# Optimization experiments

Measured on AMD Instinct MI355X. Metric: run time of the kernel, lower is better.

The kernel has to match this reference:

```python
import jax, jax.numpy as jnp
import numpy as np

INPUT_SIZE = 128
HIDDEN_SIZE = 128
B, S = 4, 4096


def setup_inputs() -> dict:
    key = jax.random.key(0)
    ks = jax.random.split(key, 9)
    sc_in = 1.0 / np.sqrt(INPUT_SIZE)
    sc_h = 1.0 / np.sqrt(HIDDEN_SIZE)
    return {
        "x": jax.random.normal(ks[0], (B, S, INPUT_SIZE), jnp.float32),
        "Wq": jax.random.uniform(ks[1], (INPUT_SIZE, HIDDEN_SIZE), jnp.float32, -sc_in, sc_in),
        "bq": jax.random.uniform(ks[2], (HIDDEN_SIZE,), jnp.float32, -sc_in, sc_in),
        "Wk": jax.random.uniform(ks[3], (INPUT_SIZE, HIDDEN_SIZE), jnp.float32, -sc_in, sc_in),
        "bk": jax.random.uniform(ks[4], (HIDDEN_SIZE,), jnp.float32, -sc_in, sc_in),
        "Wv": jax.random.uniform(ks[5], (INPUT_SIZE, HIDDEN_SIZE), jnp.float32, -sc_in, sc_in),
        "bv": jax.random.uniform(ks[6], (HIDDEN_SIZE,), jnp.float32, -sc_in, sc_in),
        "Wo": jax.random.uniform(ks[7], (HIDDEN_SIZE, INPUT_SIZE), jnp.float32, -sc_h, sc_h),
        "bo": jax.random.uniform(ks[8], (INPUT_SIZE,), jnp.float32, -sc_h, sc_h),
    }


def reference(x, Wq, bq, Wk, bk, Wv, bv, Wo, bo):
    # single-head scaled dot-product attention (non-causal), dropout is eval-mode identity
    q = x @ Wq + bq                      # [B, S, H]
    k = x @ Wk + bk                      # [B, S, H]
    v = x @ Wv + bv                      # [B, S, H]
    scale = 1.0 / jnp.sqrt(jnp.asarray(HIDDEN_SIZE, x.dtype))
    scores = jnp.einsum("bsh,bth->bst", q, k) * scale   # [B, S, S]
    attn = jax.nn.softmax(scores, axis=-1)
    attended = jnp.einsum("bst,bth->bsh", attn, v)       # [B, S, H]
    return attended @ Wo + bo                            # [B, S, input_size]
```

## Files before the change

### kernel.cpp

```cpp
#include <hip/hip_runtime.h>
#include <stdint.h>

typedef __attribute__((ext_vector_type(8))) short short8;
typedef __attribute__((ext_vector_type(4))) float f32x4;
typedef __attribute__((ext_vector_type(16))) float f32x16;
typedef __attribute__((ext_vector_type(4))) int i32x4;
typedef __attribute__((ext_vector_type(2))) int i32x2;

#define MFMA16(a, b, c) __builtin_amdgcn_mfma_f32_16x16x32_bf16((a), (b), (c), 0, 0, 0)
#define MFMA32(a, b, c) __builtin_amdgcn_mfma_f32_32x32x16_bf16((a), (b), (c), 0, 0, 0)

typedef __attribute__((address_space(1))) const void GVoid;
typedef __attribute__((address_space(3))) void LVoid;
#define GLDS16(g, l) __builtin_amdgcn_global_load_lds((GVoid*)(g), (LVoid*)(l), 16, 0, 0)

#define L2E 1.4426950408889634f

__device__ __forceinline__ unsigned short f2bf(float f) {
  unsigned int u = __builtin_bit_cast(unsigned int, f);
  u += 0x7fffu + ((u >> 16) & 1u);
  return (unsigned short)(u >> 16);
}
__device__ __forceinline__ float bf2f(unsigned short u) {
  return __builtin_bit_cast(float, (unsigned int)u << 16);
}

__device__ __forceinline__ float fexp2(float x) {
  return __builtin_amdgcn_exp2f(x);
}

__device__ __forceinline__ i32x2 pls(int a, int b) {
  return __builtin_amdgcn_permlane32_swap(a, b, false, false);
}
__device__ __forceinline__ float fasf(int x) { return __builtin_bit_cast(float, x); }
__device__ __forceinline__ int iasi(float x) { return __builtin_bit_cast(int, x); }

__device__ __forceinline__ int cvtpk(float lo, float hi) {
  int d;
  asm("v_cvt_pk_bf16_f32 %0, %1, %2" : "=v"(d) : "v"(lo), "v"(hi));
  return d;
}

__global__ __launch_bounds__(256) void k_proj(
    const float* __restrict__ x,
    const float* __restrict__ Wq, const float* __restrict__ bq,
    const float* __restrict__ Wk, const float* __restrict__ bk,
    const float* __restrict__ Wv, const float* __restrict__ bv,
    const float* __restrict__ Wo,
    unsigned short* __restrict__ Q2, unsigned short* __restrict__ K2,
    unsigned short* __restrict__ V2, unsigned short* __restrict__ Wo2)
{
  __shared__ __align__(16) unsigned short wt[128 * 128];
  __shared__ __align__(16) unsigned short st[64 * 136];
  const int tid  = threadIdx.x;
  const int lane = tid & 63;
  const int wid  = tid >> 6;
  const int l15  = lane & 15;
  const int g    = lane >> 4;
  const int wI   = blockIdx.x >> 8;
  const int blk  = blockIdx.x & 255;
  const int r0   = blk * 64 + wid * 16;

  if (blockIdx.x == 0) {
    for (int e = tid; e < 16384; e += 256) {
      int j = e & 7, ln = (e >> 3) & 63, kt = (e >> 9) & 7, dt = e >> 12;
      int h = kt * 16 + (ln >> 5) * 8 + j, oc = dt * 32 + (ln & 31);
      Wo2[e] = f2bf(Wo[h * 128 + oc]);
    }
  }

  short8 af[4];
  {
    const float* xp = x + (r0 + l15) * 128 + g * 8;
#pragma unroll
    for (int kt = 0; kt < 4; ++kt) {
      float4 v0 = *(const float4*)(xp + kt * 32);
      float4 v1 = *(const float4*)(xp + kt * 32 + 4);
      short8 a;
      a[0] = (short)f2bf(v0.x); a[1] = (short)f2bf(v0.y);
      a[2] = (short)f2bf(v0.z); a[3] = (short)f2bf(v0.w);
      a[4] = (short)f2bf(v1.x); a[5] = (short)f2bf(v1.y);
      a[6] = (short)f2bf(v1.z); a[7] = (short)f2bf(v1.w);
      af[kt] = a;
    }
  }

  const float* W  = (wI == 0) ? Wq : (wI == 1) ? Wk : Wv;
  const float* bv_ = (wI == 0) ? bq : (wI == 1) ? bk : bv;

  for (int i = 0; i < 64; ++i) {
    int idx = i * 256 + tid;
    int k = idx >> 7, n = idx & 127;
    int cs = (k >> 3) ^ (n & 7);
    wt[n * 128 + cs * 8 + (k & 7)] = f2bf(W[idx]);
  }
  __syncthreads();

  float bias[8];
#pragma unroll
  for (int nt = 0; nt < 8; ++nt) bias[nt] = bv_[nt * 16 + l15];

  f32x4 acc[8];
#pragma unroll
  for (int nt = 0; nt < 8; ++nt) acc[nt] = (f32x4){0.f, 0.f, 0.f, 0.f};

#pragma unroll
  for (int nt = 0; nt < 8; ++nt) {
    const int n = nt * 16 + l15;
#pragma unroll
    for (int ks = 0; ks < 4; ++ks) {
      int cs = (ks * 4 + g) ^ (n & 7);
      short8 bf = *(const short8*)&wt[n * 128 + cs * 8];
      acc[nt] = MFMA16(af[ks], bf, acc[nt]);
    }
  }

  if (wI < 2) {
    const float sc = (wI == 0) ? 0.08838834764831845f : 1.0f;
#pragma unroll
    for (int nt = 0; nt < 8; ++nt) {
      int col = nt * 16 + l15;
#pragma unroll
      for (int r = 0; r < 4; ++r)
        st[(wid * 16 + g * 4 + r) * 136 + col] = f2bf((acc[nt][r] + bias[nt]) * sc);
    }
    __syncthreads();
    unsigned short* Og = (wI == 0) ? Q2 : K2;
#pragma unroll
    for (int c4 = 0; c4 < 4; ++c4) {
      int c = c4 * 256 + tid;
      int T = c >> 9, cc = c & 511;
      int kt = cc >> 6, hib = (cc >> 5) & 1, s32 = cc & 31;
      int m0 = blk * 64 + T * 32;
      int bb = m0 >> 12, tile = (m0 & 4095) >> 5;
      short8 v = *(const short8*)&st[(T * 32 + s32) * 136 + kt * 16 + hib * 8];
      *(short8*)&Og[(size_t)(bb * 128 + tile) * 4096 + cc * 8] = v;
    }
  } else {
#pragma unroll
    for (int nt = 0; nt < 8; ++nt) {
      int col = nt * 16 + l15;
      int m0 = r0 + g * 4;
      int bb = m0 >> 12, srow = m0 & 4095;
      int idx = (bb * 128 + (srow >> 5)) * 4096 + ((srow >> 4) & 1) * 2048 +
                (col >> 5) * 512 + ((srow >> 3) & 1) * 256 + (col & 31) * 8 +
                (srow & 7);
      ushort4 pk;
      pk.x = f2bf(acc[nt][0] + bias[nt]);
      pk.y = f2bf(acc[nt][1] + bias[nt]);
      pk.z = f2bf(acc[nt][2] + bias[nt]);
      pk.w = f2bf(acc[nt][3] + bias[nt]);
      *(ushort4*)&V2[idx] = pk;
    }
  }
}

__global__ __launch_bounds__(256, 2) void k_attn(
    const unsigned short* __restrict__ Q2,
    const unsigned short* __restrict__ K2,
    const unsigned short* __restrict__ V2,
    unsigned short* __restrict__ PA,
    float* __restrict__ MLl)
{
  __shared__ __align__(16) char smem[65536];
  const int tid = threadIdx.x, lane = tid & 63, wid = tid >> 6;
  const int p = blockIdx.x;
  const int b = (p & 7) >> 1;
  const int idx = ((p >> 3) << 1) | (p & 1);
  const int qst = idx >> 2, kvq = idx & 3;
  const int q0tile = qst * 4 + wid;

  short8 qf[8];
  {
    const unsigned short* qp = Q2 + (size_t)(b * 128 + q0tile) * 4096 + lane * 8;
#pragma unroll
    for (int kt = 0; kt < 8; ++kt) qf[kt] = *(const short8*)(qp + kt * 512);
  }

  const unsigned short* gsrc[4];
  gsrc[0] = K2 + (size_t)(b * 128 + kvq * 32 + 0) * 4096 + tid * 8;
  gsrc[1] = K2 + (size_t)(b * 128 + kvq * 32 + 1) * 4096 + tid * 8;
  gsrc[2] = V2 + (size_t)(b * 128 + kvq * 32 + 0) * 4096 + tid * 8;
  gsrc[3] = V2 + (size_t)(b * 128 + kvq * 32 + 1) * 4096 + tid * 8;

#pragma unroll
  for (int i = 0; i < 4; ++i) {
    GLDS16(gsrc[i], smem + i * 8192 + tid * 16);
    GLDS16(gsrc[i] + 2048, smem + i * 8192 + 4096 + tid * 16);
  }

  f32x16 O[4];
#pragma unroll
  for (int dt = 0; dt < 4; ++dt)
#pragma unroll
    for (int j = 0; j < 16; ++j) O[dt][j] = 0.f;
  f32x16 zc;
#pragma unroll
  for (int j = 0; j < 16; ++j) zc[j] = 0.f;
  float lS = 0.f;

  for (int t = 0; t < 16; ++t) {
    char* const b0 = smem + (t & 1) * 32768;
    asm volatile("s_waitcnt vmcnt(0)" ::: "memory");
    __builtin_amdgcn_s_barrier();
    if (t < 15) {
      char* const bn = smem + ((t + 1) & 1) * 32768;
      const size_t adv = (size_t)(t + 1) * 8192;
#pragma unroll
      for (int i = 0; i < 4; ++i) {
        GLDS16(gsrc[i] + adv, bn + i * 8192 + tid * 16);
        GLDS16(gsrc[i] + adv + 2048, bn + i * 8192 + 4096 + tid * 16);
      }
    }
    __builtin_amdgcn_sched_barrier(0);

    f32x16 sT0, sT1;
    __builtin_amdgcn_s_setprio(1);
    {
      short8 kf[8];
#pragma unroll
      for (int kt = 0; kt < 8; ++kt)
        kf[kt] = *(const short8*)(b0 + kt * 1024 + lane * 16);
      sT0 = MFMA32(kf[0], qf[0], zc);
#pragma unroll
      for (int kt = 1; kt < 8; ++kt) sT0 = MFMA32(kf[kt], qf[kt], sT0);
    }
    {
      short8 kf[8];
#pragma unroll
      for (int kt = 0; kt < 8; ++kt)
        kf[kt] = *(const short8*)(b0 + 8192 + kt * 1024 + lane * 16);
      sT1 = MFMA32(kf[0], qf[0], zc);
#pragma unroll
      for (int kt = 1; kt < 8; ++kt) sT1 = MFMA32(kf[kt], qf[kt], sT1);
    }
    __builtin_amdgcn_s_setprio(0);

    {
      float pv[16];
#pragma unroll
      for (int r = 0; r < 16; ++r) pv[r] = fexp2(sT0[r] * L2E);
      float s01 = (pv[0] + pv[1]) + (pv[2] + pv[3]);
      float s23 = (pv[4] + pv[5]) + (pv[6] + pv[7]);
      float s45 = (pv[8] + pv[9]) + (pv[10] + pv[11]);
      float s67 = (pv[12] + pv[13]) + (pv[14] + pv[15]);
      float ts = (s01 + s23) + (s45 + s67);
      { i32x2 r = pls(iasi(ts), iasi(ts)); ts = fasf(r[0]) + fasf(r[1]); }
      lS += ts;

      short8 pa0, pa1;
      {
        int dw[8];
#pragma unroll
        for (int m = 0; m < 8; ++m) dw[m] = cvtpk(pv[2 * m], pv[2 * m + 1]);
        i32x2 ra = pls(dw[0], dw[2]);
        i32x2 rb = pls(dw[1], dw[3]);
        i32x2 rc = pls(dw[4], dw[6]);
        i32x2 rd = pls(dw[5], dw[7]);
        i32x4 w0 = {ra[0], rb[0], ra[1], rb[1]};
        i32x4 w1 = {rc[0], rd[0], rc[1], rd[1]};
        pa0 = __builtin_bit_cast(short8, w0);
        pa1 = __builtin_bit_cast(short8, w1);
      }

      __builtin_amdgcn_s_setprio(1);
      {
        const char* vb = b0 + 16384;
        short8 vf[4];
#pragma unroll
        for (int dt = 0; dt < 4; ++dt)
          vf[dt] = *(const short8*)(vb + dt * 1024 + lane * 16);
#pragma unroll
        for (int dt = 0; dt < 4; ++dt) O[dt] = MFMA32(pa0, vf[dt], O[dt]);
#pragma unroll
        for (int dt = 0; dt < 4; ++dt)
          vf[dt] = *(const short8*)(vb + 4096 + dt * 1024 + lane * 16);
#pragma unroll
        for (int dt = 0; dt < 4; ++dt) O[dt] = MFMA32(pa1, vf[dt], O[dt]);
      }
      __builtin_amdgcn_s_setprio(0);
    }

    {
      float pv[16];
#pragma unroll
      for (int r = 0; r < 16; ++r) pv[r] = fexp2(sT1[r] * L2E);
      float s01 = (pv[0] + pv[1]) + (pv[2] + pv[3]);
      float s23 = (pv[4] + pv[5]) + (pv[6] + pv[7]);
      float s45 = (pv[8] + pv[9]) + (pv[10] + pv[11]);
      float s67 = (pv[12] + pv[13]) + (pv[14] + pv[15]);
      float ts = (s01 + s23) + (s45 + s67);
      { i32x2 r = pls(iasi(ts), iasi(ts)); ts = fasf(r[0]) + fasf(r[1]); }
      lS += ts;

      short8 pa2, pa3;
      {
        int dw[8];
#pragma unroll
        for (int m = 0; m < 8; ++m) dw[m] = cvtpk(pv[2 * m], pv[2 * m + 1]);
        i32x2 ra = pls(dw[0], dw[2]);
        i32x2 rb = pls(dw[1], dw[3]);
        i32x2 rc = pls(dw[4], dw[6]);
        i32x2 rd = pls(dw[5], dw[7]);
        i32x4 w0 = {ra[0], rb[0], ra[1], rb[1]};
        i32x4 w1 = {rc[0], rd[0], rc[1], rd[1]};
        pa2 = __builtin_bit_cast(short8, w0);
        pa3 = __builtin_bit_cast(short8, w1);
      }

      __builtin_amdgcn_s_setprio(1);
      {
        const char* vb = b0 + 16384 + 8192;
        short8 vf[4];
#pragma unroll
        for (int dt = 0; dt < 4; ++dt)
          vf[dt] = *(const short8*)(vb + dt * 1024 + lane * 16);
#pragma unroll
        for (int dt = 0; dt < 4; ++dt) O[dt] = MFMA32(pa2, vf[dt], O[dt]);
#pragma unroll
        for (int dt = 0; dt < 4; ++dt)
          vf[dt] = *(const short8*)(vb + 4096 + dt * 1024 + lane * 16);
#pragma unroll
        for (int dt = 0; dt < 4; ++dt) O[dt] = MFMA32(pa3, vf[dt], O[dt]);
      }
      __builtin_amdgcn_s_setprio(0);
    }
  }

  unsigned short* pab = PA + ((size_t)(b * 4 + kvq) * 128 + q0tile) * 4096;
#pragma unroll
  for (int c = 0; c < 8; ++c) {
    int dt = c >> 1, r0 = (c & 1) * 8;
    i32x4 wv = {cvtpk(O[dt][r0 + 0], O[dt][r0 + 1]),
                cvtpk(O[dt][r0 + 2], O[dt][r0 + 3]),
                cvtpk(O[dt][r0 + 4], O[dt][r0 + 5]),
                cvtpk(O[dt][r0 + 6], O[dt][r0 + 7])};
    *(short8*)(pab + c * 512 + lane * 8) = __builtin_bit_cast(short8, wv);
  }
  if ((lane >> 5) == 0)
    MLl[(size_t)(b * 4 + kvq) * 4096 + q0tile * 32 + (lane & 31)] = lS;
}

__global__ __launch_bounds__(256) void k_merge(
    const unsigned short* __restrict__ PA,
    const float* __restrict__ MLl,
    const unsigned short* __restrict__ Wo2,
    const float* __restrict__ bo,
    float* __restrict__ out)
{
  __shared__ __align__(16) float att[8 * 64 * 8];
  const int tid = threadIdx.x, lane = tid & 63, w = tid >> 6;
  const int rr = lane & 31, hi = lane >> 5;
  const int p = blockIdx.x;
  const int b = (p & 7) >> 1;
  const int qt32 = ((p >> 3) << 1) | (p & 1);

  const int pl = lane;
  float a[2][8];
#pragma unroll
  for (int c2 = 0; c2 < 2; ++c2)
#pragma unroll
    for (int j = 0; j < 8; ++j) a[c2][j] = 0.f;
#pragma unroll
  for (int h = 0; h < 4; ++h) {
    const unsigned short* pb = PA + ((size_t)(b * 4 + h) * 128 + qt32) * 4096;
#pragma unroll
    for (int c2 = 0; c2 < 2; ++c2) {
      short8 ph = *(const short8*)(pb + (w * 2 + c2) * 512 + pl * 8);
#pragma unroll
      for (int j = 0; j < 8; ++j)
        a[c2][j] += bf2f((unsigned short)ph[j]);
    }
  }

#pragma unroll
  for (int c2 = 0; c2 < 2; ++c2) {
    int c = w * 2 + c2, dt = c >> 1;
    int kt = dt * 2 + ((pl & 31) >> 4);
    int shalf = ((pl & 31) >> 3) & 1;
    int jd = pl & 7;
#pragma unroll
    for (int j = 0; j < 8; ++j) {
      int r = (c & 1) * 8 + j;
      int row = (r & 3) + 8 * (r >> 2) + 4 * (pl >> 5);
      int s = shalf * 32 + row;
      att[kt * 512 + s * 8 + jd] = a[c2][j];
    }
  }
  __syncthreads();

  float L = 0.f;
#pragma unroll
  for (int h = 0; h < 4; ++h)
    L += MLl[(size_t)(b * 4 + h) * 4096 + qt32 * 32 + rr];
  float iL = 1.0f / L;

  short8 attb[8];
#pragma unroll
  for (int kt = 0; kt < 8; ++kt) {
    f32x4 lo = *(const f32x4*)&att[kt * 512 + lane * 8];
    f32x4 hi4 = *(const f32x4*)&att[kt * 512 + lane * 8 + 4];
    i32x4 wv = {cvtpk(lo[0] * iL, lo[1] * iL), cvtpk(lo[2] * iL, lo[3] * iL),
                cvtpk(hi4[0] * iL, hi4[1] * iL), cvtpk(hi4[2] * iL, hi4[3] * iL)};
    attb[kt] = __builtin_bit_cast(short8, wv);
  }

  short8 wof[8];
#pragma unroll
  for (int kt = 0; kt < 8; ++kt)
    wof[kt] = *(const short8*)(Wo2 + (w * 8 + kt) * 512 + lane * 8);

  f32x16 zc;
#pragma unroll
  for (int j = 0; j < 16; ++j) zc[j] = 0.f;
  f32x16 acc = MFMA32(attb[0], wof[0], zc);
#pragma unroll
  for (int kt = 1; kt < 8; ++kt) acc = MFMA32(attb[kt], wof[kt], acc);

  float bov = bo[w * 32 + rr];
  float* op = out + (size_t)(b * 4096 + qt32 * 32) * 128 + w * 32 + rr;
#pragma unroll
  for (int r = 0; r < 16; ++r) {
    int q = (r & 3) + 8 * (r >> 2) + 4 * hi;
    op[q * 128] = acc[r] + bov;
  }
}

extern "C" void kernel_launch(void* const* d_in, const int* in_sizes, int n_in,
                              void* d_out, int out_size, void* d_ws, size_t ws_size,
                              hipStream_t stream) {
  const float* x  = (const float*)d_in[0];
  const float* Wq = (const float*)d_in[1];
  const float* bq = (const float*)d_in[2];
  const float* Wk = (const float*)d_in[3];
  const float* bk = (const float*)d_in[4];
  const float* Wv = (const float*)d_in[5];
  const float* bv = (const float*)d_in[6];
  const float* Wo = (const float*)d_in[7];
  const float* bo = (const float*)d_in[8];

  const size_t NE = 4u * 4096u * 128u;
  unsigned short* Q2  = (unsigned short*)d_ws;
  unsigned short* K2  = Q2 + NE;
  unsigned short* V2  = K2 + NE;
  unsigned short* Wo2 = V2 + NE;
  unsigned short* PA  = Wo2 + 16384;
  float*          MLl = (float*)(PA + (size_t)16 * 128 * 4096);

  k_proj<<<768, 256, 0, stream>>>(x, Wq, bq, Wk, bk, Wv, bv, Wo, Q2, K2, V2, Wo2);
  k_attn<<<512, 256, 0, stream>>>(Q2, K2, V2, PA, MLl);
  k_merge<<<512, 256, 0, stream>>>(PA, MLl, Wo2, bo, (float*)d_out);
}
```

Baseline: 70.54 us.

## Give each attention wave two query tiles and split keys eight ways

Each wave now processes two 32-row query tiles against every K/V tile it stages in shared memory, so each K/V fragment read from LDS feeds twice as many MFMAs. The KV split goes from 4 to 8 chunks so the grid still has 512 blocks, and the merge kernel now sums 8 partials. This trades extra register pressure (the launch-bounds occupancy hint is removed, with two sets of accumulators and Q fragments) and twice the partial-output traffic to and from global memory for less LDS traffic per FLOP.

```diff
diff --git a/kernel.cpp b/kernel.cpp
--- a/kernel.cpp
+++ b/kernel.cpp
@@ -155,7 +155,7 @@
   }
 }
 
-__global__ __launch_bounds__(256, 2) void k_attn(
+__global__ __launch_bounds__(256) void k_attn(
     const unsigned short* __restrict__ Q2,
     const unsigned short* __restrict__ K2,
     const unsigned short* __restrict__ V2,
@@ -167,21 +167,22 @@
   const int p = blockIdx.x;
   const int b = (p & 7) >> 1;
   const int idx = ((p >> 3) << 1) | (p & 1);
-  const int qst = idx >> 2, kvq = idx & 3;
-  const int q0tile = qst * 4 + wid;
-
-  short8 qf[8];
-  {
-    const unsigned short* qp = Q2 + (size_t)(b * 128 + q0tile) * 4096 + lane * 8;
-#pragma unroll
-    for (int kt = 0; kt < 8; ++kt) qf[kt] = *(const short8*)(qp + kt * 512);
+  const int qst = idx >> 3, kvq = idx & 7;
+  const int q0A = qst * 8 + wid * 2;
+
+  short8 qf[2][8];
+#pragma unroll
+  for (int g = 0; g < 2; ++g) {
+    const unsigned short* qp = Q2 + (size_t)(b * 128 + q0A + g) * 4096 + lane * 8;
+#pragma unroll
+    for (int kt = 0; kt < 8; ++kt) qf[g][kt] = *(const short8*)(qp + kt * 512);
   }
 
   const unsigned short* gsrc[4];
-  gsrc[0] = K2 + (size_t)(b * 128 + kvq * 32 + 0) * 4096 + tid * 8;
-  gsrc[1] = K2 + (size_t)(b * 128 + kvq * 32 + 1) * 4096 + tid * 8;
-  gsrc[2] = V2 + (size_t)(b * 128 + kvq * 32 + 0) * 4096 + tid * 8;
-  gsrc[3] = V2 + (size_t)(b * 128 + kvq * 32 + 1) * 4096 + tid * 8;
+  gsrc[0] = K2 + (size_t)(b * 128 + kvq * 16 + 0) * 4096 + tid * 8;
+  gsrc[1] = K2 + (size_t)(b * 128 + kvq * 16 + 1) * 4096 + tid * 8;
+  gsrc[2] = V2 + (size_t)(b * 128 + kvq * 16 + 0) * 4096 + tid * 8;
+  gsrc[3] = V2 + (size_t)(b * 128 + kvq * 16 + 1) * 4096 + tid * 8;
 
 #pragma unroll
   for (int i = 0; i < 4; ++i) {
@@ -189,21 +190,23 @@
     GLDS16(gsrc[i] + 2048, smem + i * 8192 + 4096 + tid * 16);
   }
 
-  f32x16 O[4];
-#pragma unroll
-  for (int dt = 0; dt < 4; ++dt)
-#pragma unroll
-    for (int j = 0; j < 16; ++j) O[dt][j] = 0.f;
+  f32x16 O[2][4];
+#pragma unroll
+  for (int g = 0; g < 2; ++g)
+#pragma unroll
+    for (int dt = 0; dt < 4; ++dt)
+#pragma unroll
+      for (int j = 0; j < 16; ++j) O[g][dt][j] = 0.f;
   f32x16 zc;
 #pragma unroll
   for (int j = 0; j < 16; ++j) zc[j] = 0.f;
-  float lS = 0.f;
-
-  for (int t = 0; t < 16; ++t) {
+  float lS[2] = {0.f, 0.f};
+
+  for (int t = 0; t < 8; ++t) {
     char* const b0 = smem + (t & 1) * 32768;
     asm volatile("s_waitcnt vmcnt(0)" ::: "memory");
     __builtin_amdgcn_s_barrier();
-    if (t < 15) {
+    if (t < 7) {
       char* const bn = smem + ((t + 1) & 1) * 32768;
       const size_t adv = (size_t)(t + 1) * 8192;
 #pragma unroll
@@ -214,42 +217,40 @@
     }
     __builtin_amdgcn_sched_barrier(0);
 
-    f32x16 sT0, sT1;
-    __builtin_amdgcn_s_setprio(1);
-    {
-      short8 kf[8];
-#pragma unroll
-      for (int kt = 0; kt < 8; ++kt)
-        kf[kt] = *(const short8*)(b0 + kt * 1024 + lane * 16);
-      sT0 = MFMA32(kf[0], qf[0], zc);
-#pragma unroll
-      for (int kt = 1; kt < 8; ++kt) sT0 = MFMA32(kf[kt], qf[kt], sT0);
-    }
-    {
-      short8 kf[8];
-#pragma unroll
-      for (int kt = 0; kt < 8; ++kt)
-        kf[kt] = *(const short8*)(b0 + 8192 + kt * 1024 + lane * 16);
-      sT1 = MFMA32(kf[0], qf[0], zc);
-#pragma unroll
-      for (int kt = 1; kt < 8; ++kt) sT1 = MFMA32(kf[kt], qf[kt], sT1);
-    }
-    __builtin_amdgcn_s_setprio(0);
-
-    {
-      float pv[16];
-#pragma unroll
-      for (int r = 0; r < 16; ++r) pv[r] = fexp2(sT0[r] * L2E);
-      float s01 = (pv[0] + pv[1]) + (pv[2] + pv[3]);
-      float s23 = (pv[4] + pv[5]) + (pv[6] + pv[7]);
-      float s45 = (pv[8] + pv[9]) + (pv[10] + pv[11]);
-      float s67 = (pv[12] + pv[13]) + (pv[14] + pv[15]);
-      float ts = (s01 + s23) + (s45 + s67);
-      { i32x2 r = pls(iasi(ts), iasi(ts)); ts = fasf(r[0]) + fasf(r[1]); }
-      lS += ts;
-
-      short8 pa0, pa1;
+#pragma unroll
+    for (int half = 0; half < 2; ++half) {
+      const char* kb = b0 + half * 8192;
+      const char* vb = b0 + 16384 + half * 8192;
+
+      f32x16 sTa, sTb;
+      __builtin_amdgcn_s_setprio(1);
       {
+        short8 kf[8];
+#pragma unroll
+        for (int kt = 0; kt < 8; ++kt)
+          kf[kt] = *(const short8*)(kb + kt * 1024 + lane * 16);
+        sTa = MFMA32(kf[0], qf[0][0], zc);
+        sTb = MFMA32(kf[0], qf[1][0], zc);
+#pragma unroll
+        for (int kt = 1; kt < 8; ++kt) {
+          sTa = MFMA32(kf[kt], qf[0][kt], sTa);
+          sTb = MFMA32(kf[kt], qf[1][kt], sTb);
+        }
+      }
+      __builtin_amdgcn_s_setprio(0);
+
+      short8 paA0, paA1, paB0, paB1;
+      {
+        float pv[16];
+#pragma unroll
+        for (int r = 0; r < 16; ++r) pv[r] = fexp2(sTa[r] * L2E);
+        float s01 = (pv[0] + pv[1]) + (pv[2] + pv[3]);
+        float s23 = (pv[4] + pv[5]) + (pv[6] + pv[7]);
+        float s45 = (pv[8] + pv[9]) + (pv[10] + pv[11]);
+        float s67 = (pv[12] + pv[13]) + (pv[14] + pv[15]);
+        float ts = (s01 + s23) + (s45 + s67);
+        { i32x2 r = pls(iasi(ts), iasi(ts)); ts = fasf(r[0]) + fasf(r[1]); }
+        lS[0] += ts;
         int dw[8];
 #pragma unroll
         for (int m = 0; m < 8; ++m) dw[m] = cvtpk(pv[2 * m], pv[2 * m + 1]);
@@ -259,42 +260,20 @@
         i32x2 rd = pls(dw[5], dw[7]);
         i32x4 w0 = {ra[0], rb[0], ra[1], rb[1]};
         i32x4 w1 = {rc[0], rd[0], rc[1], rd[1]};
-        pa0 = __builtin_bit_cast(short8, w0);
-        pa1 = __builtin_bit_cast(short8, w1);
+        paA0 = __builtin_bit_cast(short8, w0);
+        paA1 = __builtin_bit_cast(short8, w1);
       }
-
-      __builtin_amdgcn_s_setprio(1);
       {
-        const char* vb = b0 + 16384;
-        short8 vf[4];
-#pragma unroll
-        for (int dt = 0; dt < 4; ++dt)
-          vf[dt] = *(const short8*)(vb + dt * 1024 + lane * 16);
-#pragma unroll
-        for (int dt = 0; dt < 4; ++dt) O[dt] = MFMA32(pa0, vf[dt], O[dt]);
-#pragma unroll
-        for (int dt = 0; dt < 4; ++dt)
-          vf[dt] = *(const short8*)(vb + 4096 + dt * 1024 + lane * 16);
-#pragma unroll
-        for (int dt = 0; dt < 4; ++dt) O[dt] = MFMA32(pa1, vf[dt], O[dt]);
-      }
-      __builtin_amdgcn_s_setprio(0);
-    }
-
-    {
-      float pv[16];
-#pragma unroll
-      for (int r = 0; r < 16; ++r) pv[r] = fexp2(sT1[r] * L2E);
-      float s01 = (pv[0] + pv[1]) + (pv[2] + pv[3]);
-      float s23 = (pv[4] + pv[5]) + (pv[6] + pv[7]);
-      float s45 = (pv[8] + pv[9]) + (pv[10] + pv[11]);
-      float s67 = (pv[12] + pv[13]) + (pv[14] + pv[15]);
-      float ts = (s01 + s23) + (s45 + s67);
-      { i32x2 r = pls(iasi(ts), iasi(ts)); ts = fasf(r[0]) + fasf(r[1]); }
-      lS += ts;
-
-      short8 pa2, pa3;
-      {
+        float pv[16];
+#pragma unroll
+        for (int r = 0; r < 16; ++r) pv[r] = fexp2(sTb[r] * L2E);
+        float s01 = (pv[0] + pv[1]) + (pv[2] + pv[3]);
+        float s23 = (pv[4] + pv[5]) + (pv[6] + pv[7]);
+        float s45 = (pv[8] + pv[9]) + (pv[10] + pv[11]);
+        float s67 = (pv[12] + pv[13]) + (pv[14] + pv[15]);
+        float ts = (s01 + s23) + (s45 + s67);
+        { i32x2 r = pls(iasi(ts), iasi(ts)); ts = fasf(r[0]) + fasf(r[1]); }
+        lS[1] += ts;
         int dw[8];
 #pragma unroll
         for (int m = 0; m < 8; ++m) dw[m] = cvtpk(pv[2 * m], pv[2 * m + 1]);
@@ -304,41 +283,49 @@
         i32x2 rd = pls(dw[5], dw[7]);
         i32x4 w0 = {ra[0], rb[0], ra[1], rb[1]};
         i32x4 w1 = {rc[0], rd[0], rc[1], rd[1]};
-        pa2 = __builtin_bit_cast(short8, w0);
-        pa3 = __builtin_bit_cast(short8, w1);
+        paB0 = __builtin_bit_cast(short8, w0);
+        paB1 = __builtin_bit_cast(short8, w1);
       }
 
       __builtin_amdgcn_s_setprio(1);
       {
-        const char* vb = b0 + 16384 + 8192;
         short8 vf[4];
 #pragma unroll
         for (int dt = 0; dt < 4; ++dt)
           vf[dt] = *(const short8*)(vb + dt * 1024 + lane * 16);
 #pragma unroll
-        for (int dt = 0; dt < 4; ++dt) O[dt] = MFMA32(pa2, vf[dt], O[dt]);
+        for (int dt = 0; dt < 4; ++dt) {
+          O[0][dt] = MFMA32(paA0, vf[dt], O[0][dt]);
+          O[1][dt] = MFMA32(paB0, vf[dt], O[1][dt]);
+        }
 #pragma unroll
         for (int dt = 0; dt < 4; ++dt)
           vf[dt] = *(const short8*)(vb + 4096 + dt * 1024 + lane * 16);
 #pragma unroll
-        for (int dt = 0; dt < 4; ++dt) O[dt] = MFMA32(pa3, vf[dt], O[dt]);
+        for (int dt = 0; dt < 4; ++dt) {
+          O[0][dt] = MFMA32(paA1, vf[dt], O[0][dt]);
+          O[1][dt] = MFMA32(paB1, vf[dt], O[1][dt]);
+        }
       }
       __builtin_amdgcn_s_setprio(0);
     }
   }
 
-  unsigned short* pab = PA + ((size_t)(b * 4 + kvq) * 128 + q0tile) * 4096;
-#pragma unroll
-  for (int c = 0; c < 8; ++c) {
-    int dt = c >> 1, r0 = (c & 1) * 8;
-    i32x4 wv = {cvtpk(O[dt][r0 + 0], O[dt][r0 + 1]),
-                cvtpk(O[dt][r0 + 2], O[dt][r0 + 3]),
-                cvtpk(O[dt][r0 + 4], O[dt][r0 + 5]),
-                cvtpk(O[dt][r0 + 6], O[dt][r0 + 7])};
-    *(short8*)(pab + c * 512 + lane * 8) = __builtin_bit_cast(short8, wv);
-  }
-  if ((lane >> 5) == 0)
-    MLl[(size_t)(b * 4 + kvq) * 4096 + q0tile * 32 + (lane & 31)] = lS;
+#pragma unroll
+  for (int g = 0; g < 2; ++g) {
+    unsigned short* pab = PA + ((size_t)(b * 8 + kvq) * 128 + q0A + g) * 4096;
+#pragma unroll
+    for (int c = 0; c < 8; ++c) {
+      int dt = c >> 1, r0 = (c & 1) * 8;
+      i32x4 wv = {cvtpk(O[g][dt][r0 + 0], O[g][dt][r0 + 1]),
+                  cvtpk(O[g][dt][r0 + 2], O[g][dt][r0 + 3]),
+                  cvtpk(O[g][dt][r0 + 4], O[g][dt][r0 + 5]),
+                  cvtpk(O[g][dt][r0 + 6], O[g][dt][r0 + 7])};
+      *(short8*)(pab + c * 512 + lane * 8) = __builtin_bit_cast(short8, wv);
+    }
+    if ((lane >> 5) == 0)
+      MLl[(size_t)(b * 8 + kvq) * 4096 + (q0A + g) * 32 + (lane & 31)] = lS[g];
+  }
 }
 
 __global__ __launch_bounds__(256) void k_merge(
@@ -362,8 +349,8 @@
 #pragma unroll
     for (int j = 0; j < 8; ++j) a[c2][j] = 0.f;
 #pragma unroll
-  for (int h = 0; h < 4; ++h) {
-    const unsigned short* pb = PA + ((size_t)(b * 4 + h) * 128 + qt32) * 4096;
+  for (int h = 0; h < 8; ++h) {
+    const unsigned short* pb = PA + ((size_t)(b * 8 + h) * 128 + qt32) * 4096;
 #pragma unroll
     for (int c2 = 0; c2 < 2; ++c2) {
       short8 ph = *(const short8*)(pb + (w * 2 + c2) * 512 + pl * 8);
@@ -391,8 +378,8 @@
 
   float L = 0.f;
 #pragma unroll
-  for (int h = 0; h < 4; ++h)
-    L += MLl[(size_t)(b * 4 + h) * 4096 + qt32 * 32 + rr];
+  for (int h = 0; h < 8; ++h)
+    L += MLl[(size_t)(b * 8 + h) * 4096 + qt32 * 32 + rr];
   float iL = 1.0f / L;
 
   short8 attb[8];
@@ -445,7 +432,7 @@
   unsigned short* V2  = K2 + NE;
   unsigned short* Wo2 = V2 + NE;
   unsigned short* PA  = Wo2 + 16384;
-  float*          MLl = (float*)(PA + (size_t)16 * 128 * 4096);
+  float*          MLl = (float*)(PA + (size_t)32 * 128 * 4096);
 
   k_proj<<<768, 256, 0, stream>>>(x, Wq, bq, Wk, bk, Wv, bv, Wo, Q2, K2, V2, Wo2);
   k_attn<<<512, 256, 0, stream>>>(Q2, K2, V2, PA, MLl);
```

After: 79.14 us. 1.12x slower.

## Quantize Q and K to FP8 and use FP8 MFMA for attention scores

Applied to the files above, without the earlier changes.

Q and K projections are now stored as FP8 (e4m3) instead of bf16, and the QK^T score computation uses the 32x32x16 fp8 MFMA. The softmax scale moves from the Q projection into the exp2 multiplier, K tiles in LDS halve in size, and the shared buffer shrinks. This targets QK MFMA throughput, K/Q memory traffic and LDS footprint, at the cost of reduced score precision. Q/K values are unscaled, which risks FP8 range and accuracy issues.

```diff
diff --git a/kernel.cpp b/kernel.cpp
--- a/kernel.cpp
+++ b/kernel.cpp
@@ -9,12 +9,14 @@
 
 #define MFMA16(a, b, c) __builtin_amdgcn_mfma_f32_16x16x32_bf16((a), (b), (c), 0, 0, 0)
 #define MFMA32(a, b, c) __builtin_amdgcn_mfma_f32_32x32x16_bf16((a), (b), (c), 0, 0, 0)
+#define MFMA8(a, b, c)  __builtin_amdgcn_mfma_f32_32x32x16_fp8_fp8((a), (b), (c), 0, 0, 0)
 
 typedef __attribute__((address_space(1))) const void GVoid;
 typedef __attribute__((address_space(3))) void LVoid;
 #define GLDS16(g, l) __builtin_amdgcn_global_load_lds((GVoid*)(g), (LVoid*)(l), 16, 0, 0)
 
 #define L2E 1.4426950408889634f
+#define SCL (1.4426950408889634f * 0.08838834764831845f)
 
 __device__ __forceinline__ unsigned short f2bf(float f) {
   unsigned int u = __builtin_bit_cast(unsigned int, f);
@@ -47,7 +49,7 @@
     const float* __restrict__ Wk, const float* __restrict__ bk,
     const float* __restrict__ Wv, const float* __restrict__ bv,
     const float* __restrict__ Wo,
-    unsigned short* __restrict__ Q2, unsigned short* __restrict__ K2,
+    uint8_t* __restrict__ Q8, uint8_t* __restrict__ K8,
     unsigned short* __restrict__ V2, unsigned short* __restrict__ Wo2)
 {
   __shared__ __align__(16) unsigned short wt[128 * 128];
@@ -116,16 +118,15 @@
   }
 
   if (wI < 2) {
-    const float sc = (wI == 0) ? 0.08838834764831845f : 1.0f;
 #pragma unroll
     for (int nt = 0; nt < 8; ++nt) {
       int col = nt * 16 + l15;
 #pragma unroll
       for (int r = 0; r < 4; ++r)
-        st[(wid * 16 + g * 4 + r) * 136 + col] = f2bf((acc[nt][r] + bias[nt]) * sc);
+        st[(wid * 16 + g * 4 + r) * 136 + col] = f2bf(acc[nt][r] + bias[nt]);
     }
     __syncthreads();
-    unsigned short* Og = (wI == 0) ? Q2 : K2;
+    uint8_t* Og = (wI == 0) ? Q8 : K8;
 #pragma unroll
     for (int c4 = 0; c4 < 4; ++c4) {
       int c = c4 * 256 + tid;
@@ -134,7 +135,17 @@
       int m0 = blk * 64 + T * 32;
       int bb = m0 >> 12, tile = (m0 & 4095) >> 5;
       short8 v = *(const short8*)&st[(T * 32 + s32) * 136 + kt * 16 + hib * 8];
-      *(short8*)&Og[(size_t)(bb * 128 + tile) * 4096 + cc * 8] = v;
+      int lo = 0, hi = 0;
+      lo = __builtin_amdgcn_cvt_pk_fp8_f32(bf2f((unsigned short)v[0]),
+                                           bf2f((unsigned short)v[1]), lo, false);
+      lo = __builtin_amdgcn_cvt_pk_fp8_f32(bf2f((unsigned short)v[2]),
+                                           bf2f((unsigned short)v[3]), lo, true);
+      hi = __builtin_amdgcn_cvt_pk_fp8_f32(bf2f((unsigned short)v[4]),
+                                           bf2f((unsigned short)v[5]), hi, false);
+      hi = __builtin_amdgcn_cvt_pk_fp8_f32(bf2f((unsigned short)v[6]),
+                                           bf2f((unsigned short)v[7]), hi, true);
+      int2 pk8; pk8.x = lo; pk8.y = hi;
+      *(int2*)&Og[(size_t)(bb * 128 + tile) * 4096 + cc * 8] = pk8;
     }
   } else {
 #pragma unroll
@@ -156,13 +167,13 @@
 }
 
 __global__ __launch_bounds__(256, 2) void k_attn(
-    const unsigned short* __restrict__ Q2,
-    const unsigned short* __restrict__ K2,
+    const uint8_t* __restrict__ Q8,
+    const uint8_t* __restrict__ K8,
     const unsigned short* __restrict__ V2,
     unsigned short* __restrict__ PA,
     float* __restrict__ MLl)
 {
-  __shared__ __align__(16) char smem[65536];
+  __shared__ __align__(16) char smem[49152];
   const int tid = threadIdx.x, lane = tid & 63, wid = tid >> 6;
   const int p = blockIdx.x;
   const int b = (p & 7) >> 1;
@@ -170,24 +181,23 @@
   const int qst = idx >> 2, kvq = idx & 3;
   const int q0tile = qst * 4 + wid;
 
-  short8 qf[8];
+  long qf[8];
   {
-    const unsigned short* qp = Q2 + (size_t)(b * 128 + q0tile) * 4096 + lane * 8;
-#pragma unroll
-    for (int kt = 0; kt < 8; ++kt) qf[kt] = *(const short8*)(qp + kt * 512);
-  }
-
-  const unsigned short* gsrc[4];
-  gsrc[0] = K2 + (size_t)(b * 128 + kvq * 32 + 0) * 4096 + tid * 8;
-  gsrc[1] = K2 + (size_t)(b * 128 + kvq * 32 + 1) * 4096 + tid * 8;
-  gsrc[2] = V2 + (size_t)(b * 128 + kvq * 32 + 0) * 4096 + tid * 8;
-  gsrc[3] = V2 + (size_t)(b * 128 + kvq * 32 + 1) * 4096 + tid * 8;
-
-#pragma unroll
-  for (int i = 0; i < 4; ++i) {
-    GLDS16(gsrc[i], smem + i * 8192 + tid * 16);
-    GLDS16(gsrc[i] + 2048, smem + i * 8192 + 4096 + tid * 16);
-  }
+    const uint8_t* qp = Q8 + (size_t)(b * 128 + q0tile) * 4096 + lane * 8;
+#pragma unroll
+    for (int kt = 0; kt < 8; ++kt) qf[kt] = *(const long*)(qp + kt * 512);
+  }
+
+  const uint8_t* k8s = K8 + (size_t)(b * 128 + kvq * 32) * 4096 + tid * 16;
+  const unsigned short* v0s = V2 + (size_t)(b * 128 + kvq * 32 + 0) * 4096 + tid * 8;
+  const unsigned short* v1s = V2 + (size_t)(b * 128 + kvq * 32 + 1) * 4096 + tid * 8;
+
+  GLDS16(k8s,         smem + tid * 16);
+  GLDS16(k8s + 4096,  smem + 4096 + tid * 16);
+  GLDS16(v0s,         smem + 8192 + tid * 16);
+  GLDS16(v0s + 2048,  smem + 12288 + tid * 16);
+  GLDS16(v1s,         smem + 16384 + tid * 16);
+  GLDS16(v1s + 2048,  smem + 20480 + tid * 16);
 
   f32x16 O[4];
 #pragma unroll
@@ -200,46 +210,47 @@
   float lS = 0.f;
 
   for (int t = 0; t < 16; ++t) {
-    char* const b0 = smem + (t & 1) * 32768;
+    char* const b0 = smem + (t & 1) * 24576;
     asm volatile("s_waitcnt vmcnt(0)" ::: "memory");
     __builtin_amdgcn_s_barrier();
     if (t < 15) {
-      char* const bn = smem + ((t + 1) & 1) * 32768;
+      char* const bn = smem + ((t + 1) & 1) * 24576;
       const size_t adv = (size_t)(t + 1) * 8192;
-#pragma unroll
-      for (int i = 0; i < 4; ++i) {
-        GLDS16(gsrc[i] + adv, bn + i * 8192 + tid * 16);
-        GLDS16(gsrc[i] + adv + 2048, bn + i * 8192 + 4096 + tid * 16);
-      }
+      GLDS16(k8s + adv,        bn + tid * 16);
+      GLDS16(k8s + adv + 4096, bn + 4096 + tid * 16);
+      GLDS16(v0s + adv,        bn + 8192 + tid * 16);
+      GLDS16(v0s + adv + 2048, bn + 12288 + tid * 16);
+      GLDS16(v1s + adv,        bn + 16384 + tid * 16);
+      GLDS16(v1s + adv + 2048, bn + 20480 + tid * 16);
     }
     __builtin_amdgcn_sched_barrier(0);
 
     f32x16 sT0, sT1;
     __builtin_amdgcn_s_setprio(1);
     {
-      short8 kf[8];
+      long kf[8];
 #pragma unroll
       for (int kt = 0; kt < 8; ++kt)
-        kf[kt] = *(const short8*)(b0 + kt * 1024 + lane * 16);
-      sT0 = MFMA32(kf[0], qf[0], zc);
-#pragma unroll
-      for (int kt = 1; kt < 8; ++kt) sT0 = MFMA32(kf[kt], qf[kt], sT0);
+        kf[kt] = *(const long*)(b0 + kt * 512 + lane * 8);
+      sT0 = MFMA8(kf[0], qf[0], zc);
+#pragma unroll
+      for (int kt = 1; kt < 8; ++kt) sT0 = MFMA8(kf[kt], qf[kt], sT0);
     }
     {
-      short8 kf[8];
+      long kf[8];
 #pragma unroll
       for (int kt = 0; kt < 8; ++kt)
-        kf[kt] = *(const short8*)(b0 + 8192 + kt * 1024 + lane * 16);
-      sT1 = MFMA32(kf[0], qf[0], zc);
-#pragma unroll
-      for (int kt = 1; kt < 8; ++kt) sT1 = MFMA32(kf[kt], qf[kt], sT1);
+        kf[kt] = *(const long*)(b0 + 4096 + kt * 512 + lane * 8);
+      sT1 = MFMA8(kf[0], qf[0], zc);
+#pragma unroll
+      for (int kt = 1; kt < 8; ++kt) sT1 = MFMA8(kf[kt], qf[kt], sT1);
     }
     __builtin_amdgcn_s_setprio(0);
 
     {
       float pv[16];
 #pragma unroll
-      for (int r = 0; r < 16; ++r) pv[r] = fexp2(sT0[r] * L2E);
+      for (int r = 0; r < 16; ++r) pv[r] = fexp2(sT0[r] * SCL);
       float s01 = (pv[0] + pv[1]) + (pv[2] + pv[3]);
       float s23 = (pv[4] + pv[5]) + (pv[6] + pv[7]);
       float s45 = (pv[8] + pv[9]) + (pv[10] + pv[11]);
@@ -265,7 +276,7 @@
 
       __builtin_amdgcn_s_setprio(1);
       {
-        const char* vb = b0 + 16384;
+        const char* vb = b0 + 8192;
         short8 vf[4];
 #pragma unroll
         for (int dt = 0; dt < 4; ++dt)
@@ -284,7 +295,7 @@
     {
       float pv[16];
 #pragma unroll
-      for (int r = 0; r < 16; ++r) pv[r] = fexp2(sT1[r] * L2E);
+      for (int r = 0; r < 16; ++r) pv[r] = fexp2(sT1[r] * SCL);
       float s01 = (pv[0] + pv[1]) + (pv[2] + pv[3]);
       float s23 = (pv[4] + pv[5]) + (pv[6] + pv[7]);
       float s45 = (pv[8] + pv[9]) + (pv[10] + pv[11]);
@@ -310,7 +321,7 @@
 
       __builtin_amdgcn_s_setprio(1);
       {
-        const char* vb = b0 + 16384 + 8192;
+        const char* vb = b0 + 16384;
         short8 vf[4];
 #pragma unroll
         for (int dt = 0; dt < 4; ++dt)
@@ -440,14 +451,14 @@
   const float* bo = (const float*)d_in[8];
 
   const size_t NE = 4u * 4096u * 128u;
-  unsigned short* Q2  = (unsigned short*)d_ws;
-  unsigned short* K2  = Q2 + NE;
-  unsigned short* V2  = K2 + NE;
+  uint8_t*        Q8  = (uint8_t*)d_ws;
+  uint8_t*        K8  = Q8 + NE;
+  unsigned short* V2  = (unsigned short*)(K8 + NE);
   unsigned short* Wo2 = V2 + NE;
   unsigned short* PA  = Wo2 + 16384;
   float*          MLl = (float*)(PA + (size_t)16 * 128 * 4096);
 
-  k_proj<<<768, 256, 0, stream>>>(x, Wq, bq, Wk, bk, Wv, bv, Wo, Q2, K2, V2, Wo2);
-  k_attn<<<512, 256, 0, stream>>>(Q2, K2, V2, PA, MLl);
+  k_proj<<<768, 256, 0, stream>>>(x, Wq, bq, Wk, bk, Wv, bv, Wo, Q8, K8, V2, Wo2);
+  k_attn<<<512, 256, 0, stream>>>(Q8, K8, V2, PA, MLl);
   k_merge<<<512, 256, 0, stream>>>(PA, MLl, Wo2, bo, (float*)d_out);
 }
```

Result: faster. 66.46 us (-5.8%).
